# Optimization experiments

Measured on AMD Instinct MI355X. Metric: run time of the kernel, lower is better.

The kernel has to match this reference:

```python
import jax, jax.numpy as jnp
import numpy as np

D_MODEL = 512
NUM_HEADS = 8
DEPTH = D_MODEL // NUM_HEADS


def setup_inputs() -> dict:
    key = jax.random.key(0)
    kx, kq, kk, kv, ko = jax.random.split(key, 5)
    B, S = 2, 4096
    X = jax.random.normal(kx, (B, S, D_MODEL), dtype=jnp.float32)
    # Dense(use_bias=False) kernels: [in, out]
    scale = 1.0 / np.sqrt(D_MODEL)
    Wq = jax.random.normal(kq, (D_MODEL, D_MODEL), dtype=jnp.float32) * scale
    Wk = jax.random.normal(kk, (D_MODEL, D_MODEL), dtype=jnp.float32) * scale
    Wv = jax.random.normal(kv, (D_MODEL, D_MODEL), dtype=jnp.float32) * scale
    Wo = jax.random.normal(ko, (D_MODEL, D_MODEL), dtype=jnp.float32) * scale
    return {"X": X, "Wq": Wq, "Wk": Wk, "Wv": Wv, "Wo": Wo}


def reference(X, Wq, Wk, Wv, Wo):
    B, S, _ = X.shape
    H, Dh = NUM_HEADS, DEPTH

    def split_heads(t):  # [B,S,D] -> [B,H,S,Dh]
        return t.reshape(B, S, H, Dh).transpose(0, 2, 1, 3)

    Qh = split_heads(X @ Wq)
    Kh = split_heads(X @ Wk)
    Vh = split_heads(X @ Wv)

    inv_scale = 1.0 / jnp.sqrt(jnp.float32(Dh))
    scores = jnp.einsum('bhqd,bhkd->bhqk', Qh, Kh) * inv_scale
    attn = jax.nn.softmax(scores, axis=-1)
    context = jnp.einsum('bhqk,bhkd->bhqd', attn, Vh)
    combined = context.transpose(0, 2, 1, 3).reshape(B, S, H * Dh)
    return combined @ Wo
```

## Files before the change

### kernel.cpp

```cpp
#include <hip/hip_runtime.h>

#define D_MODEL 512
#define NHEADS 8
#define DH 64
#define BATCH 2
#define SEQ 4096
#define MTOT (BATCH*SEQ)

typedef __attribute__((ext_vector_type(8))) short bf16x8;
typedef __attribute__((ext_vector_type(4))) short s16x4;
typedef __attribute__((ext_vector_type(4))) float f32x4;

__device__ __forceinline__ unsigned short f2b(float f) {
  unsigned int u = __float_as_uint(f);
  u = (u + 0x7fffu + ((u >> 16) & 1u)) >> 16;
  return (unsigned short)u;
}

__device__ __forceinline__ float fexp2(float x) {
  return __builtin_amdgcn_exp2f(x);
}

__device__ __forceinline__ unsigned int cvtpk_bf16(float a, float b) {
  unsigned int r;
  asm("v_cvt_pk_bf16_f32 %0, %1, %2" : "=v"(r) : "v"(a), "v"(b));
  return r;
}

__device__ __forceinline__ void tr16(unsigned addr, s16x4& d) {
  asm volatile("ds_read_b64_tr_b16 %0, %1" : "=v"(d) : "v"(addr));
}


__global__ void cvt_x_kernel(const float* __restrict__ X,
                             unsigned short* __restrict__ Xb, int n) {
  int i = (blockIdx.x * blockDim.x + threadIdx.x) * 8;
  if (i >= n) return;
  const float4* s = (const float4*)(X + i);
  float4 v0 = s[0], v1 = s[1];
  union { bf16x8 v; unsigned short u[8]; } r;
  r.u[0] = f2b(v0.x); r.u[1] = f2b(v0.y); r.u[2] = f2b(v0.z); r.u[3] = f2b(v0.w);
  r.u[4] = f2b(v1.x); r.u[5] = f2b(v1.y); r.u[6] = f2b(v1.z); r.u[7] = f2b(v1.w);
  *(bf16x8*)(Xb + i) = r.v;
}

__global__ void cvt_w_kernel(const float* __restrict__ W0, const float* __restrict__ W1,
                             const float* __restrict__ W2, const float* __restrict__ W3,
                             unsigned short* __restrict__ Wt) {
  const float* Ws[4] = {W0, W1, W2, W3};
  const float* W = Ws[blockIdx.y];
  int t = blockIdx.x * blockDim.x + threadIdx.x;
  int k = t >> 9, n = t & 511;
  Wt[(size_t)blockIdx.y * (512*512) + (size_t)n * 512 + k] = f2b(W[t]);
}

__global__ __launch_bounds__(256) void gemm128_kernel(
    const unsigned short* __restrict__ A,
    const unsigned short* __restrict__ WtAll,
    unsigned short* __restrict__ qkv,
    float* __restrict__ outF,
    int modeParam) {
  int mode = (modeParam < 0) ? (int)blockIdx.z : modeParam;
  const unsigned short* Wt = WtAll + (size_t)((modeParam < 0) ? blockIdx.z : 0) * (512*512);

  __shared__ __align__(16) unsigned short Alds[128][72];
  __shared__ __align__(16) unsigned short Blds[128][72];

  int t = threadIdx.x;
  int lane = t & 63, wave = t >> 6;
  int wr = wave >> 1, wc = wave & 1;
  int lr = lane & 15, lg = lane >> 4;
  int mBase = blockIdx.x * 128;
  int nBase = blockIdx.y * 128;

  f32x4 zero = {0.f, 0.f, 0.f, 0.f};
  f32x4 acc[4][4];
#pragma unroll
  for (int i = 0; i < 4; i++)
#pragma unroll
    for (int j = 0; j < 4; j++) acc[i][j] = zero;

  int seg = t & 7, r0 = t >> 3;

  for (int k0 = 0; k0 < 512; k0 += 64) {
#pragma unroll
    for (int p = 0; p < 4; ++p) {
      int row = r0 + p * 32;
      *(int4*)&Alds[row][seg * 8] =
          *(const int4*)(A + (size_t)(mBase + row) * 512 + k0 + seg * 8);
      *(int4*)&Blds[row][seg * 8] =
          *(const int4*)(Wt + (size_t)(nBase + row) * 512 + k0 + seg * 8);
    }
    __syncthreads();
#pragma unroll
    for (int kk = 0; kk < 64; kk += 32) {
      bf16x8 afr[4], bfr[4];
#pragma unroll
      for (int mi = 0; mi < 4; mi++)
        afr[mi] = *(const bf16x8*)&Alds[wr * 64 + mi * 16 + lr][kk + lg * 8];
#pragma unroll
      for (int ni = 0; ni < 4; ni++)
        bfr[ni] = *(const bf16x8*)&Blds[wc * 64 + ni * 16 + lr][kk + lg * 8];
#pragma unroll
      for (int mi = 0; mi < 4; mi++)
#pragma unroll
        for (int ni = 0; ni < 4; ni++)
          acc[mi][ni] = __builtin_amdgcn_mfma_f32_16x16x32_bf16(
              afr[mi], bfr[ni], acc[mi][ni], 0, 0, 0);
    }
    __syncthreads();
  }

#pragma unroll
  for (int mi = 0; mi < 4; mi++) {
#pragma unroll
    for (int ni = 0; ni < 4; ni++) {
#pragma unroll
      for (int rg = 0; rg < 4; rg++) {
        int r = mBase + wr * 64 + mi * 16 + lg * 4 + rg;
        int c = nBase + wc * 64 + ni * 16 + lr;
        float v = acc[mi][ni][rg];
        if (mode < 3) {
          int b = r >> 12, s = r & 4095, h = c >> 6, d = c & 63;
          qkv[(size_t)mode * ((size_t)MTOT * 512) +
              ((((size_t)b * NHEADS + h) * SEQ + s) * DH + d)] = f2b(v);
        } else {
          outF[(size_t)r * 512 + c] = v;
        }
      }
    }
  }
}

__global__ __launch_bounds__(512) void attn_kernel(
    const unsigned short* __restrict__ Qb,
    const unsigned short* __restrict__ Kb,
    const unsigned short* __restrict__ Vb,
    unsigned short* __restrict__ CTX) {
  int flat = blockIdx.x;
  int xcd = flat & 7, jj = flat >> 3;
  int bh = xcd + ((jj >> 5) << 3);
  int qc = jj & 31;
  int b = bh >> 3, h = bh & 7;
  const unsigned short* Qp = Qb + (size_t)bh * SEQ * DH;
  const unsigned short* Kp = Kb + (size_t)bh * SEQ * DH;
  const unsigned short* Vp = Vb + (size_t)bh * SEQ * DH;

  __shared__ __align__(128) unsigned short Kl[2][64][72];
  __shared__ __align__(128) unsigned short Vl[2][4096];
  __shared__ __align__(128) unsigned short PT[8][16][72];

  int t = threadIdx.x;
  int lane = t & 63, wave = t >> 6;
  int lr = lane & 15, lg = lane >> 4;
  int q0 = qc * 128 + wave * 16;

  bf16x8 aq[2];
#pragma unroll
  for (int kk = 0; kk < 2; ++kk)
    aq[kk] = *(const bf16x8*)(Qp + (size_t)(q0 + lr) * DH + kk * 32 + lg * 8);

  f32x4 zero = {0.f, 0.f, 0.f, 0.f};
  f32x4 o[4];
#pragma unroll
  for (int dt = 0; dt < 4; dt++) o[dt] = zero;
  float m2 = -1e30f, lsum = 0.f;

  const float c2 = 0.125f * 1.44269504088896340736f;

  int srow = t >> 3, sseg = t & 7;
  int vdst = ((srow >> 2) * 4 + (sseg >> 1)) * 64 + (srow & 3) * 16 + (sseg & 1) * 8;
  const int NT = SEQ / 64;

  unsigned vtr_lane = (unsigned)(lg * 1024 + lr * 8);
  unsigned vbuf0 = (unsigned)(size_t)&Vl[0][0];
  unsigned vbuf1 = (unsigned)(size_t)&Vl[1][0];

  int4 kreg = *(const int4*)(Kp + (size_t)srow * DH + sseg * 8);
  int4 vreg = *(const int4*)(Vp + (size_t)srow * DH + sseg * 8);

  for (int kb = 0; kb < NT; ++kb) {
    int cur = kb & 1;
    *(int4*)&Kl[cur][srow][sseg * 8] = kreg;
    *(int4*)&Vl[cur][vdst] = vreg;
    if (kb + 1 < NT) {
      kreg = *(const int4*)(Kp + (size_t)((kb + 1) * 64 + srow) * DH + sseg * 8);
      vreg = *(const int4*)(Vp + (size_t)((kb + 1) * 64 + srow) * DH + sseg * 8);
    }
    __syncthreads();

    f32x4 sacc[4];
    __builtin_amdgcn_s_setprio(1);
#pragma unroll
    for (int nt = 0; nt < 4; nt++) {
      sacc[nt] = zero;
#pragma unroll
      for (int kk = 0; kk < 2; kk++) {
        bf16x8 bk = *(const bf16x8*)&Kl[cur][nt * 16 + lr][kk * 32 + lg * 8];
        sacc[nt] = __builtin_amdgcn_mfma_f32_16x16x32_bf16(bk, aq[kk], sacc[nt], 0, 0, 0);
      }
    }
    __builtin_amdgcn_s_setprio(0);

    float pm;
    {
      float a0 = fmaxf(fmaxf(sacc[0][0], sacc[0][1]), fmaxf(sacc[0][2], sacc[0][3]));
      float a1 = fmaxf(fmaxf(sacc[1][0], sacc[1][1]), fmaxf(sacc[1][2], sacc[1][3]));
      float a2 = fmaxf(fmaxf(sacc[2][0], sacc[2][1]), fmaxf(sacc[2][2], sacc[2][3]));
      float a3 = fmaxf(fmaxf(sacc[3][0], sacc[3][1]), fmaxf(sacc[3][2], sacc[3][3]));
      pm = fmaxf(fmaxf(a0, a1), fmaxf(a2, a3)) * c2;
    }
    pm = fmaxf(pm, __shfl_xor(pm, 16));
    pm = fmaxf(pm, __shfl_xor(pm, 32));

    if (!__all((int)(pm <= m2 + 8.f))) {
      float mn = fmaxf(m2, pm);
      float corr = fexp2(m2 - mn);
      m2 = mn;
      lsum *= corr;
#pragma unroll
      for (int dt = 0; dt < 4; dt++) {
        f32x4 tmp = o[dt];
        tmp[0] *= corr; tmp[1] *= corr; tmp[2] *= corr; tmp[3] *= corr;
        o[dt] = tmp;
      }
    }

    float p[4][4];
    float rs = 0.f;
#pragma unroll
    for (int nt = 0; nt < 4; nt++)
#pragma unroll
      for (int r = 0; r < 4; r++) {
        float v = fexp2(fmaf(sacc[nt][r], c2, -m2));
        p[nt][r] = v;
        rs += v;
      }
    rs += __shfl_xor(rs, 16);
    rs += __shfl_xor(rs, 32);
    lsum += rs;

#pragma unroll
    for (int nt = 0; nt < 4; nt++) {
      uint2 w;
      w.x = cvtpk_bf16(p[nt][0], p[nt][1]);
      w.y = cvtpk_bf16(p[nt][2], p[nt][3]);
      *(uint2*)&PT[wave][lr][nt * 16 + lg * 4] = w;
    }

    bf16x8 ap[2];
#pragma unroll
    for (int ks = 0; ks < 2; ks++)
      ap[ks] = *(const bf16x8*)&PT[wave][lr][ks * 32 + lg * 8];

    unsigned vb = (cur ? vbuf1 : vbuf0) + vtr_lane;
    union { bf16x8 v; s16x4 hh[2]; } bv[4][2];
#pragma unroll
    for (int dt = 0; dt < 4; dt++)
#pragma unroll
      for (int ks = 0; ks < 2; ks++) {
        tr16(vb + ks * 4096 + 0 * 512 + dt * 128, bv[dt][ks].hh[0]);
        tr16(vb + ks * 4096 + 1 * 512 + dt * 128, bv[dt][ks].hh[1]);
      }
    asm volatile("s_waitcnt lgkmcnt(0)" ::: "memory");
    __builtin_amdgcn_sched_barrier(0);
    __builtin_amdgcn_s_setprio(1);
#pragma unroll
    for (int dt = 0; dt < 4; dt++)
#pragma unroll
      for (int ks = 0; ks < 2; ks++)
        o[dt] = __builtin_amdgcn_mfma_f32_16x16x32_bf16(bv[dt][ks].v, ap[ks], o[dt], 0, 0, 0);
    __builtin_amdgcn_s_setprio(0);
  }

  float inv = 1.f / lsum;
#pragma unroll
  for (int dt = 0; dt < 4; dt++) {
    uint2 w;
    w.x = cvtpk_bf16(o[dt][0] * inv, o[dt][1] * inv);
    w.y = cvtpk_bf16(o[dt][2] * inv, o[dt][3] * inv);
    *(uint2*)&PT[wave][lr][dt * 16 + lg * 4] = w;
  }

  int row = lane >> 2, cs = lane & 3;
  bf16x8 w0 = *(const bf16x8*)&PT[wave][row][cs * 16];
  bf16x8 w1 = *(const bf16x8*)&PT[wave][row][cs * 16 + 8];
  size_t base = ((size_t)(b * SEQ + q0 + row)) * 512 + h * 64 + cs * 16;
  *(bf16x8*)(CTX + base) = w0;
  *(bf16x8*)(CTX + base + 8) = w1;
}


extern "C" void kernel_launch(void* const* d_in, const int* in_sizes, int n_in,
                              void* d_out, int out_size, void* d_ws, size_t ws_size,
                              hipStream_t stream) {
  const float* X  = (const float*)d_in[0];
  const float* Wq = (const float*)d_in[1];
  const float* Wk = (const float*)d_in[2];
  const float* Wv = (const float*)d_in[3];
  const float* Wo = (const float*)d_in[4];
  float* out = (float*)d_out;

  char* ws = (char*)d_ws;
  unsigned short* Wqt = (unsigned short*)(ws);
  unsigned short* Wot = (unsigned short*)(ws + 3u * 524288u);
  unsigned short* Xb  = (unsigned short*)(ws + 4u * 524288u);
  unsigned short* Qb  = (unsigned short*)(ws + 4u * 524288u + 8388608u);
  unsigned short* Kb  = Qb + (size_t)MTOT * 512;
  unsigned short* Vb  = Kb + (size_t)MTOT * 512;
  unsigned short* CTX = Vb + (size_t)MTOT * 512;

  int nX = MTOT * D_MODEL;
  cvt_x_kernel<<<dim3(nX / (8 * 256)), dim3(256), 0, stream>>>(X, Xb, nX);
  cvt_w_kernel<<<dim3(1024, 4), dim3(256), 0, stream>>>(Wq, Wk, Wv, Wo, Wqt);
  gemm128_kernel<<<dim3(64, 4, 3), dim3(256), 0, stream>>>(Xb, Wqt, Qb, nullptr, -1);
  attn_kernel<<<dim3(512), dim3(512), 0, stream>>>(Qb, Kb, Vb, CTX);
  gemm128_kernel<<<dim3(64, 4, 1), dim3(256), 0, stream>>>(CTX, Wot, nullptr, out, 3);
}
```

Baseline: 189.3 us.

## Switch attention to 32x32x16 MFMA with 32 queries per wave, 4 waves

The attention kernel now gives each wave 32 query rows instead of 16 and uses 32x32x16 bf16 MFMA for both QK^T and PV in place of 16x16x32. The block drops to 256 threads (4 waves), so each thread stages two K/V rows per tile. The P staging buffer and output write-back are re-laid out to match. The larger MFMA tile and fewer waves mean each K/V tile in shared memory feeds more math per load and the number of cross-lane reductions drops. The cost is more registers per thread (16-wide accumulators) and fewer waves per block to hide latency.

```diff
diff --git a/kernel.cpp b/kernel.cpp
--- a/kernel.cpp
+++ b/kernel.cpp
@@ -10,6 +10,7 @@
 typedef __attribute__((ext_vector_type(8))) short bf16x8;
 typedef __attribute__((ext_vector_type(4))) short s16x4;
 typedef __attribute__((ext_vector_type(4))) float f32x4;
+typedef __attribute__((ext_vector_type(16))) float f32x16;
 
 __device__ __forceinline__ unsigned short f2b(float f) {
   unsigned int u = __float_as_uint(f);
@@ -132,7 +133,7 @@
   }
 }
 
-__global__ __launch_bounds__(512) void attn_kernel(
+__global__ __launch_bounds__(256) void attn_kernel(
     const unsigned short* __restrict__ Qb,
     const unsigned short* __restrict__ Kb,
     const unsigned short* __restrict__ Vb,
@@ -148,69 +149,86 @@
 
   __shared__ __align__(128) unsigned short Kl[2][64][72];
   __shared__ __align__(128) unsigned short Vl[2][4096];
-  __shared__ __align__(128) unsigned short PT[8][16][72];
+  __shared__ __align__(128) unsigned short PT[4][32][72];
 
   int t = threadIdx.x;
   int lane = t & 63, wave = t >> 6;
-  int lr = lane & 15, lg = lane >> 4;
-  int q0 = qc * 128 + wave * 16;
-
-  bf16x8 aq[2];
-#pragma unroll
-  for (int kk = 0; kk < 2; ++kk)
-    aq[kk] = *(const bf16x8*)(Qp + (size_t)(q0 + lr) * DH + kk * 32 + lg * 8);
-
-  f32x4 zero = {0.f, 0.f, 0.f, 0.f};
-  f32x4 o[4];
-#pragma unroll
-  for (int dt = 0; dt < 4; dt++) o[dt] = zero;
+  int q = lane & 31, hv = lane >> 5;
+  int lr = lane & 15, lg2 = (lane >> 4) & 1;
+  int q0w = qc * 128 + wave * 32;
+
+  bf16x8 aq[4];
+#pragma unroll
+  for (int s = 0; s < 4; s++)
+    aq[s] = *(const bf16x8*)(Qp + (size_t)(q0w + q) * DH + s * 16 + hv * 8);
+
+  f32x16 o0, o1;
+#pragma unroll
+  for (int i = 0; i < 16; i++) { o0[i] = 0.f; o1[i] = 0.f; }
   float m2 = -1e30f, lsum = 0.f;
 
   const float c2 = 0.125f * 1.44269504088896340736f;
 
   int srow = t >> 3, sseg = t & 7;
-  int vdst = ((srow >> 2) * 4 + (sseg >> 1)) * 64 + (srow & 3) * 16 + (sseg & 1) * 8;
   const int NT = SEQ / 64;
 
-  unsigned vtr_lane = (unsigned)(lg * 1024 + lr * 8);
+  unsigned vtr_lane = (unsigned)(hv * 1024 + lg2 * 128 + lr * 8);
   unsigned vbuf0 = (unsigned)(size_t)&Vl[0][0];
   unsigned vbuf1 = (unsigned)(size_t)&Vl[1][0];
 
-  int4 kreg = *(const int4*)(Kp + (size_t)srow * DH + sseg * 8);
-  int4 vreg = *(const int4*)(Vp + (size_t)srow * DH + sseg * 8);
+  int4 kreg[2], vreg[2];
+#pragma unroll
+  for (int p = 0; p < 2; ++p) {
+    int row = srow + p * 32;
+    kreg[p] = *(const int4*)(Kp + (size_t)row * DH + sseg * 8);
+    vreg[p] = *(const int4*)(Vp + (size_t)row * DH + sseg * 8);
+  }
 
   for (int kb = 0; kb < NT; ++kb) {
     int cur = kb & 1;
-    *(int4*)&Kl[cur][srow][sseg * 8] = kreg;
-    *(int4*)&Vl[cur][vdst] = vreg;
+#pragma unroll
+    for (int p = 0; p < 2; ++p) {
+      int row = srow + p * 32;
+      *(int4*)&Kl[cur][row][sseg * 8] = kreg[p];
+      int vdst = ((row >> 2) * 4 + (sseg >> 1)) * 64 + (row & 3) * 16 + (sseg & 1) * 8;
+      *(int4*)&Vl[cur][vdst] = vreg[p];
+    }
     if (kb + 1 < NT) {
-      kreg = *(const int4*)(Kp + (size_t)((kb + 1) * 64 + srow) * DH + sseg * 8);
-      vreg = *(const int4*)(Vp + (size_t)((kb + 1) * 64 + srow) * DH + sseg * 8);
+#pragma unroll
+      for (int p = 0; p < 2; ++p) {
+        int row = srow + p * 32;
+        kreg[p] = *(const int4*)(Kp + (size_t)((kb + 1) * 64 + row) * DH + sseg * 8);
+        vreg[p] = *(const int4*)(Vp + (size_t)((kb + 1) * 64 + row) * DH + sseg * 8);
+      }
     }
     __syncthreads();
 
-    f32x4 sacc[4];
+    f32x16 s0, s1;
+#pragma unroll
+    for (int i = 0; i < 16; i++) { s0[i] = 0.f; s1[i] = 0.f; }
     __builtin_amdgcn_s_setprio(1);
 #pragma unroll
-    for (int nt = 0; nt < 4; nt++) {
-      sacc[nt] = zero;
-#pragma unroll
-      for (int kk = 0; kk < 2; kk++) {
-        bf16x8 bk = *(const bf16x8*)&Kl[cur][nt * 16 + lr][kk * 32 + lg * 8];
-        sacc[nt] = __builtin_amdgcn_mfma_f32_16x16x32_bf16(bk, aq[kk], sacc[nt], 0, 0, 0);
-      }
+    for (int s = 0; s < 4; s++) {
+      bf16x8 bk0 = *(const bf16x8*)&Kl[cur][q][s * 16 + hv * 8];
+      bf16x8 bk1 = *(const bf16x8*)&Kl[cur][32 + q][s * 16 + hv * 8];
+      s0 = __builtin_amdgcn_mfma_f32_32x32x16_bf16(bk0, aq[s], s0, 0, 0, 0);
+      s1 = __builtin_amdgcn_mfma_f32_32x32x16_bf16(bk1, aq[s], s1, 0, 0, 0);
     }
     __builtin_amdgcn_s_setprio(0);
 
     float pm;
     {
-      float a0 = fmaxf(fmaxf(sacc[0][0], sacc[0][1]), fmaxf(sacc[0][2], sacc[0][3]));
-      float a1 = fmaxf(fmaxf(sacc[1][0], sacc[1][1]), fmaxf(sacc[1][2], sacc[1][3]));
-      float a2 = fmaxf(fmaxf(sacc[2][0], sacc[2][1]), fmaxf(sacc[2][2], sacc[2][3]));
-      float a3 = fmaxf(fmaxf(sacc[3][0], sacc[3][1]), fmaxf(sacc[3][2], sacc[3][3]));
-      pm = fmaxf(fmaxf(a0, a1), fmaxf(a2, a3)) * c2;
-    }
-    pm = fmaxf(pm, __shfl_xor(pm, 16));
+      float a0 = fmaxf(fmaxf(s0[0], s0[1]), fmaxf(s0[2], s0[3]));
+      float a1 = fmaxf(fmaxf(s0[4], s0[5]), fmaxf(s0[6], s0[7]));
+      float a2 = fmaxf(fmaxf(s0[8], s0[9]), fmaxf(s0[10], s0[11]));
+      float a3 = fmaxf(fmaxf(s0[12], s0[13]), fmaxf(s0[14], s0[15]));
+      float b0 = fmaxf(fmaxf(s1[0], s1[1]), fmaxf(s1[2], s1[3]));
+      float b1 = fmaxf(fmaxf(s1[4], s1[5]), fmaxf(s1[6], s1[7]));
+      float b2 = fmaxf(fmaxf(s1[8], s1[9]), fmaxf(s1[10], s1[11]));
+      float b3 = fmaxf(fmaxf(s1[12], s1[13]), fmaxf(s1[14], s1[15]));
+      pm = fmaxf(fmaxf(fmaxf(a0, a1), fmaxf(a2, a3)),
+                 fmaxf(fmaxf(b0, b1), fmaxf(b2, b3))) * c2;
+    }
     pm = fmaxf(pm, __shfl_xor(pm, 32));
 
     if (!__all((int)(pm <= m2 + 8.f))) {
@@ -219,75 +237,88 @@
       m2 = mn;
       lsum *= corr;
 #pragma unroll
-      for (int dt = 0; dt < 4; dt++) {
-        f32x4 tmp = o[dt];
-        tmp[0] *= corr; tmp[1] *= corr; tmp[2] *= corr; tmp[3] *= corr;
-        o[dt] = tmp;
-      }
-    }
-
-    float p[4][4];
+      for (int i = 0; i < 16; i++) { o0[i] *= corr; o1[i] *= corr; }
+    }
+
     float rs = 0.f;
 #pragma unroll
-    for (int nt = 0; nt < 4; nt++)
-#pragma unroll
-      for (int r = 0; r < 4; r++) {
-        float v = fexp2(fmaf(sacc[nt][r], c2, -m2));
-        p[nt][r] = v;
-        rs += v;
-      }
-    rs += __shfl_xor(rs, 16);
+    for (int rg = 0; rg < 4; rg++) {
+      float p0 = fexp2(fmaf(s0[rg * 4 + 0], c2, -m2));
+      float p1 = fexp2(fmaf(s0[rg * 4 + 1], c2, -m2));
+      float p2 = fexp2(fmaf(s0[rg * 4 + 2], c2, -m2));
+      float p3 = fexp2(fmaf(s0[rg * 4 + 3], c2, -m2));
+      rs += (p0 + p1) + (p2 + p3);
+      uint2 w; w.x = cvtpk_bf16(p0, p1); w.y = cvtpk_bf16(p2, p3);
+      *(uint2*)&PT[wave][q][rg * 8 + hv * 4] = w;
+      float q0_ = fexp2(fmaf(s1[rg * 4 + 0], c2, -m2));
+      float q1_ = fexp2(fmaf(s1[rg * 4 + 1], c2, -m2));
+      float q2_ = fexp2(fmaf(s1[rg * 4 + 2], c2, -m2));
+      float q3_ = fexp2(fmaf(s1[rg * 4 + 3], c2, -m2));
+      rs += (q0_ + q1_) + (q2_ + q3_);
+      uint2 w2; w2.x = cvtpk_bf16(q0_, q1_); w2.y = cvtpk_bf16(q2_, q3_);
+      *(uint2*)&PT[wave][q][32 + rg * 8 + hv * 4] = w2;
+    }
     rs += __shfl_xor(rs, 32);
     lsum += rs;
 
-#pragma unroll
-    for (int nt = 0; nt < 4; nt++) {
-      uint2 w;
-      w.x = cvtpk_bf16(p[nt][0], p[nt][1]);
-      w.y = cvtpk_bf16(p[nt][2], p[nt][3]);
-      *(uint2*)&PT[wave][lr][nt * 16 + lg * 4] = w;
-    }
-
-    bf16x8 ap[2];
-#pragma unroll
-    for (int ks = 0; ks < 2; ks++)
-      ap[ks] = *(const bf16x8*)&PT[wave][lr][ks * 32 + lg * 8];
+    bf16x8 ap[4];
+#pragma unroll
+    for (int s = 0; s < 4; s++)
+      ap[s] = *(const bf16x8*)&PT[wave][q][s * 16 + hv * 8];
 
     unsigned vb = (cur ? vbuf1 : vbuf0) + vtr_lane;
-    union { bf16x8 v; s16x4 hh[2]; } bv[4][2];
-#pragma unroll
-    for (int dt = 0; dt < 4; dt++)
-#pragma unroll
-      for (int ks = 0; ks < 2; ks++) {
-        tr16(vb + ks * 4096 + 0 * 512 + dt * 128, bv[dt][ks].hh[0]);
-        tr16(vb + ks * 4096 + 1 * 512 + dt * 128, bv[dt][ks].hh[1]);
+    {
+      union { bf16x8 v; s16x4 hh[2]; } bv[4];
+#pragma unroll
+      for (int s = 0; s < 4; s++) {
+        tr16(vb + s * 2048 + 0 * 512 + 0 * 256, bv[s].hh[0]);
+        tr16(vb + s * 2048 + 1 * 512 + 0 * 256, bv[s].hh[1]);
       }
-    asm volatile("s_waitcnt lgkmcnt(0)" ::: "memory");
-    __builtin_amdgcn_sched_barrier(0);
-    __builtin_amdgcn_s_setprio(1);
-#pragma unroll
-    for (int dt = 0; dt < 4; dt++)
-#pragma unroll
-      for (int ks = 0; ks < 2; ks++)
-        o[dt] = __builtin_amdgcn_mfma_f32_16x16x32_bf16(bv[dt][ks].v, ap[ks], o[dt], 0, 0, 0);
-    __builtin_amdgcn_s_setprio(0);
+      asm volatile("s_waitcnt lgkmcnt(0)" ::: "memory");
+      __builtin_amdgcn_sched_barrier(0);
+      __builtin_amdgcn_s_setprio(1);
+#pragma unroll
+      for (int s = 0; s < 4; s++)
+        o0 = __builtin_amdgcn_mfma_f32_32x32x16_bf16(bv[s].v, ap[s], o0, 0, 0, 0);
+      __builtin_amdgcn_s_setprio(0);
+    }
+    {
+      union { bf16x8 v; s16x4 hh[2]; } bv[4];
+#pragma unroll
+      for (int s = 0; s < 4; s++) {
+        tr16(vb + s * 2048 + 0 * 512 + 1 * 256, bv[s].hh[0]);
+        tr16(vb + s * 2048 + 1 * 512 + 1 * 256, bv[s].hh[1]);
+      }
+      asm volatile("s_waitcnt lgkmcnt(0)" ::: "memory");
+      __builtin_amdgcn_sched_barrier(0);
+      __builtin_amdgcn_s_setprio(1);
+#pragma unroll
+      for (int s = 0; s < 4; s++)
+        o1 = __builtin_amdgcn_mfma_f32_32x32x16_bf16(bv[s].v, ap[s], o1, 0, 0, 0);
+      __builtin_amdgcn_s_setprio(0);
+    }
   }
 
   float inv = 1.f / lsum;
 #pragma unroll
-  for (int dt = 0; dt < 4; dt++) {
+  for (int rg = 0; rg < 4; rg++) {
     uint2 w;
-    w.x = cvtpk_bf16(o[dt][0] * inv, o[dt][1] * inv);
-    w.y = cvtpk_bf16(o[dt][2] * inv, o[dt][3] * inv);
-    *(uint2*)&PT[wave][lr][dt * 16 + lg * 4] = w;
-  }
-
-  int row = lane >> 2, cs = lane & 3;
-  bf16x8 w0 = *(const bf16x8*)&PT[wave][row][cs * 16];
-  bf16x8 w1 = *(const bf16x8*)&PT[wave][row][cs * 16 + 8];
-  size_t base = ((size_t)(b * SEQ + q0 + row)) * 512 + h * 64 + cs * 16;
-  *(bf16x8*)(CTX + base) = w0;
-  *(bf16x8*)(CTX + base + 8) = w1;
+    w.x = cvtpk_bf16(o0[rg * 4 + 0] * inv, o0[rg * 4 + 1] * inv);
+    w.y = cvtpk_bf16(o0[rg * 4 + 2] * inv, o0[rg * 4 + 3] * inv);
+    *(uint2*)&PT[wave][q][rg * 8 + hv * 4] = w;
+    uint2 w2;
+    w2.x = cvtpk_bf16(o1[rg * 4 + 0] * inv, o1[rg * 4 + 1] * inv);
+    w2.y = cvtpk_bf16(o1[rg * 4 + 2] * inv, o1[rg * 4 + 3] * inv);
+    *(uint2*)&PT[wave][q][32 + rg * 8 + hv * 4] = w2;
+  }
+
+  int qr = lane >> 1, half = lane & 1;
+  size_t base = ((size_t)(b * SEQ + q0w + qr)) * 512 + h * 64 + half * 32;
+#pragma unroll
+  for (int i = 0; i < 4; i++) {
+    bf16x8 w = *(const bf16x8*)&PT[wave][qr][half * 32 + i * 8];
+    *(bf16x8*)(CTX + base + i * 8) = w;
+  }
 }
 
 
@@ -314,6 +345,6 @@
   cvt_x_kernel<<<dim3(nX / (8 * 256)), dim3(256), 0, stream>>>(X, Xb, nX);
   cvt_w_kernel<<<dim3(1024, 4), dim3(256), 0, stream>>>(Wq, Wk, Wv, Wo, Wqt);
   gemm128_kernel<<<dim3(64, 4, 3), dim3(256), 0, stream>>>(Xb, Wqt, Qb, nullptr, -1);
-  attn_kernel<<<dim3(512), dim3(512), 0, stream>>>(Qb, Kb, Vb, CTX);
+  attn_kernel<<<dim3(512), dim3(256), 0, stream>>>(Qb, Kb, Vb, CTX);
   gemm128_kernel<<<dim3(64, 4, 1), dim3(256), 0, stream>>>(CTX, Wot, nullptr, out, 3);
 }
```

New measurement: 212.4 us. 12.2% more time.
